# Kernel tuning notes

Measured on AMD Instinct MI355X. Metric: run time of the kernel, lower is better.

Reference implementation:

```python
import jax, jax.numpy as jnp
import numpy as np

K = 20
EPS = 1e-5


def _knn_idx(x, k):
    # x: (B, C, N) -> idx (B, N, k) of nearest neighbors (largest negative sq dist)
    xt = jnp.swapaxes(x, 1, 2)                      # (B, N, C)
    inner = -2.0 * jnp.einsum('bnc,bmc->bnm', xt, xt)
    xx = jnp.sum(x * x, axis=1)                      # (B, N)
    pd = -xx[:, :, None] - inner - xx[:, None, :]    # (B, N, N)
    return jax.lax.top_k(pd, k)[1]


def _graph_feature(x, k):
    # x: (B, C, N) -> (B, 2C, N, k): concat(neighbor - center, center)
    idx = _knn_idx(x, k)                             # (B, N, k) int
    xt = jnp.swapaxes(x, 1, 2)                       # (B, N, C)
    neigh = jax.vmap(lambda f, i: f[i])(xt, idx)     # (B, N, k, C)
    center = jnp.broadcast_to(xt[:, :, None, :], neigh.shape)
    feat = jnp.concatenate([neigh - center, center], axis=-1)  # (B, N, k, 2C)
    return jnp.transpose(feat, (0, 3, 1, 2))         # (B, 2C, N, k)


def _bn_lrelu(y, g, b, rm, rv, chan_axis_nd):
    # inference-mode batchnorm per channel (dim 1) followed by LeakyReLU(0.2)
    shp = [1, -1] + [1] * chan_axis_nd
    scale = (g / jnp.sqrt(rv + EPS)).reshape(shp)
    y = (y - rm.reshape(shp)) * scale + b.reshape(shp)
    return jnp.where(y > 0, y, 0.2 * y)


def _edge_block(x, w, g, b, rm, rv):
    f = _graph_feature(x, K)                          # (B, 2C, N, k)
    y = jnp.einsum('oc,bcnk->bonk', w, f)            # conv2d 1x1, no bias
    y = _bn_lrelu(y, g, b, rm, rv, 2)
    return jnp.max(y, axis=-1)                       # max over k -> (B, O, N)


def setup_inputs() -> dict:
    key = jax.random.key(0)
    ks = jax.random.split(key, 32)
    B, N = 8, 4096
    d = {'x': jax.random.normal(ks[0], (B, 1, N), jnp.float32)}
    wshapes = {'w1': (64, 2), 'w2': (64, 128), 'w3': (128, 128), 'w4': (256, 256),
               'w5': (1024, 512), 'wreg': (1, 1024)}
    i = 1
    for name, s in wshapes.items():
        d[name] = jax.random.normal(ks[i], s, jnp.float32) * 0.1
        i += 1
    chans = {'1': 64, '2': 64, '3': 128, '4': 256, '5': 1024}
    for tag, c in chans.items():
        d['g' + tag] = 1.0 + 0.1 * jax.random.normal(ks[i], (c,), jnp.float32); i += 1
        d['b' + tag] = 0.1 * jax.random.normal(ks[i], (c,), jnp.float32); i += 1
        d['rm' + tag] = 0.1 * jax.random.normal(ks[i], (c,), jnp.float32); i += 1
        d['rv' + tag] = jax.random.uniform(ks[i], (c,), jnp.float32, 0.5, 1.5); i += 1
    return d


def reference(x, w1, w2, w3, w4, w5, wreg,
              g1, b1, rm1, rv1, g2, b2, rm2, rv2, g3, b3, rm3, rv3,
              g4, b4, rm4, rv4, g5, b5, rm5, rv5):
    x1 = _edge_block(x, w1, g1, b1, rm1, rv1)        # (B, 64, N)
    x2 = _edge_block(x1, w2, g2, b2, rm2, rv2)       # (B, 64, N)
    x3 = _edge_block(x2, w3, g3, b3, rm3, rv3)       # (B, 128, N)
    x4 = _edge_block(x3, w4, g4, b4, rm4, rv4)       # (B, 256, N)
    h = jnp.concatenate([x1, x2, x3, x4], axis=1)    # (B, 512, N)
    h = jnp.einsum('oc,bcn->bon', w5, h)             # conv1d 1x1 -> (B, 1024, N)
    h = _bn_lrelu(h, g5, b5, rm5, rv5, 1)
    return jnp.einsum('oc,bcn->bon', wreg, h)        # (B, 1, N)
```

## Files before the change

kernel.cpp:

```cpp
#include <hip/hip_runtime.h>
#include <math.h>


constexpr int NPT = 4096;
constexpr int BATCH = 8;
constexpr int PTS = BATCH * NPT;
constexpr float EPS = 1e-5f;
#define KC 16
#define PAD 68
#define PADB 132
#define NEG_INF -3.4e38f

typedef __attribute__((ext_vector_type(8))) short bf16x8;
typedef __attribute__((ext_vector_type(4))) float f32x4;

__device__ __forceinline__ ushort f2bf(float f) {
    unsigned u = __float_as_uint(f);
    return (ushort)((u + 0x7fffu + ((u >> 16) & 1u)) >> 16);
}

__global__ __launch_bounds__(256) void sqnorm(const float* __restrict__ X,
                                              float* __restrict__ xx, int C) {
    int p = blockIdx.x * 256 + threadIdx.x;
    if (p >= PTS) return;
    float s = 0.f;
    const float* row = X + (size_t)p * C;
    for (int c = 0; c < C; ++c) s = fmaf(row[c], row[c], s);
    xx[p] = s;
}

__global__ __launch_bounds__(256) void sqnorm_cvt(const float* __restrict__ X,
                                                  float* __restrict__ xx,
                                                  ushort* __restrict__ Xh,
                                                  ushort* __restrict__ Xl, int C) {
    int p = blockIdx.x * 256 + threadIdx.x;
    if (p >= PTS) return;
    const float* row = X + (size_t)p * C;
    ushort* hr = Xh + (size_t)p * C;
    ushort* lr = Xl + (size_t)p * C;
    float s = 0.f;
    for (int c = 0; c < C; ++c) {
        float v = row[c];
        s = fmaf(v, v, s);
        ushort hb = f2bf(v);
        float hf = __uint_as_float((unsigned)hb << 16);
        hr[c] = hb;
        lr[c] = f2bf(v - hf);
    }
    xx[p] = s;
}

__global__ __launch_bounds__(256) void pd_mfma(const ushort* __restrict__ Xh,
                                               const ushort* __restrict__ Xl,
                                               const float* __restrict__ xx,
                                               float* __restrict__ pd0,
                                               int C, int bbase, size_t pdstride) {
    int b = bbase + blockIdx.y;
    float* pd = pd0 + (size_t)blockIdx.y * pdstride;
    int bid = blockIdx.x;
    int ti = 0, rem = bid;
    while (rem >= 32 - ti) { rem -= 32 - ti; ++ti; }
    int tj = ti + rem;
    int rowbase = ti * 128, colbase = tj * 128;
    int p0 = b * NPT;

    __shared__ ushort Rh[128][40], Rl[128][40], Ch[128][40], Cl[128][40];
    __shared__ float xxr[128], xxc[128];
    int tid = threadIdx.x;
    int lane = tid & 63, wid = tid >> 6;
    int wr = wid >> 1, wc = wid & 1;

    if (tid < 128) xxr[tid] = xx[p0 + rowbase + tid];
    else           xxc[tid - 128] = xx[p0 + colbase + tid - 128];

    const int pt = tid >> 1;
    const int co = (tid & 1) * 16;
    size_t rrow = (size_t)(p0 + rowbase + pt) * C;
    size_t crow = (size_t)(p0 + colbase + pt) * C;

    f32x4 z = {0.f, 0.f, 0.f, 0.f};
    f32x4 acc[4][4];
#pragma unroll
    for (int sr = 0; sr < 4; ++sr)
#pragma unroll
        for (int sc = 0; sc < 4; ++sc) acc[sr][sc] = z;

    for (int c0 = 0; c0 < C; c0 += 32) {
        uint4 vrh0 = *(const uint4*)&Xh[rrow + c0 + co];
        uint4 vrh1 = *(const uint4*)&Xh[rrow + c0 + co + 8];
        uint4 vrl0 = *(const uint4*)&Xl[rrow + c0 + co];
        uint4 vrl1 = *(const uint4*)&Xl[rrow + c0 + co + 8];
        uint4 vch0 = *(const uint4*)&Xh[crow + c0 + co];
        uint4 vch1 = *(const uint4*)&Xh[crow + c0 + co + 8];
        uint4 vcl0 = *(const uint4*)&Xl[crow + c0 + co];
        uint4 vcl1 = *(const uint4*)&Xl[crow + c0 + co + 8];
        __syncthreads();
        *(uint4*)&Rh[pt][co] = vrh0; *(uint4*)&Rh[pt][co + 8] = vrh1;
        *(uint4*)&Rl[pt][co] = vrl0; *(uint4*)&Rl[pt][co + 8] = vrl1;
        *(uint4*)&Ch[pt][co] = vch0; *(uint4*)&Ch[pt][co + 8] = vch1;
        *(uint4*)&Cl[pt][co] = vcl0; *(uint4*)&Cl[pt][co + 8] = vcl1;
        __syncthreads();
        bf16x8 ah[4], al[4], bh[4], bl[4];
#pragma unroll
        for (int s = 0; s < 4; ++s) {
            int ar = wr * 64 + s * 16 + (lane & 15);
            int br = wc * 64 + s * 16 + (lane & 15);
            int ko = (lane >> 4) * 8;
            ah[s] = *(const bf16x8*)&Rh[ar][ko];
            al[s] = *(const bf16x8*)&Rl[ar][ko];
            bh[s] = *(const bf16x8*)&Ch[br][ko];
            bl[s] = *(const bf16x8*)&Cl[br][ko];
        }
#pragma unroll
        for (int sr = 0; sr < 4; ++sr)
#pragma unroll
            for (int sc = 0; sc < 4; ++sc) {
                acc[sr][sc] = __builtin_amdgcn_mfma_f32_16x16x32_bf16(ah[sr], bh[sc], acc[sr][sc], 0, 0, 0);
                acc[sr][sc] = __builtin_amdgcn_mfma_f32_16x16x32_bf16(ah[sr], bl[sc], acc[sr][sc], 0, 0, 0);
                acc[sr][sc] = __builtin_amdgcn_mfma_f32_16x16x32_bf16(al[sr], bh[sc], acc[sr][sc], 0, 0, 0);
            }
    }

    int rl0 = wr * 64 + (lane >> 4) * 4;
    int ml  = wc * 64 + (lane & 15);
#pragma unroll
    for (int sr = 0; sr < 4; ++sr)
#pragma unroll
        for (int sc = 0; sc < 4; ++sc) {
            int mm = ml + sc * 16;
            float xm = xxc[mm];
#pragma unroll
            for (int reg = 0; reg < 4; ++reg) {
                int rr = rl0 + sr * 16 + reg;
                float o = 2.f * acc[sr][sc][reg] - xxr[rr] - xm;
                pd[(size_t)(rowbase + rr) * NPT + colbase + mm] = o;
            }
        }
    if (ti != tj) {
#pragma unroll
        for (int sr = 0; sr < 4; ++sr) {
            int rr0 = rl0 + sr * 16;
#pragma unroll
            for (int sc = 0; sc < 4; ++sc) {
                int mm = ml + sc * 16;
                float xm = xxc[mm];
                float4 o;
                o.x = 2.f * acc[sr][sc][0] - xm - xxr[rr0 + 0];
                o.y = 2.f * acc[sr][sc][1] - xm - xxr[rr0 + 1];
                o.z = 2.f * acc[sr][sc][2] - xm - xxr[rr0 + 2];
                o.w = 2.f * acc[sr][sc][3] - xm - xxr[rr0 + 3];
                *(float4*)&pd[(size_t)(colbase + mm) * NPT + rowbase + rr0] = o;
            }
        }
    }
}

__device__ __forceinline__ void topk_core(float (&v)[64], int lane, int b,
                                          int* __restrict__ op) {
    float m1 = NEG_INF, m2 = NEG_INF;
    int j1 = 0, j2 = 0;
#pragma unroll
    for (int j = 0; j < 64; ++j) {
        float vv = v[j];
        bool c1 = vv > m1;
        bool c2 = vv > m2;
        m2 = c1 ? m1 : (c2 ? vv : m2);
        j2 = c1 ? j1 : (c2 ? j : j2);
        m1 = c1 ? vv : m1;
        j1 = c1 ? j : j1;
    }
    bool have2 = true;
    unsigned long long remM = 0ull;
    for (int t = 0; t < 20; ++t) {
        int g1 = ((j1 >> 2) << 8) + (lane << 2) + (j1 & 3);
        float bv = m1; int gi = g1;
#pragma unroll
        for (int s = 1; s < 64; s <<= 1) {
            float ov = __shfl_xor(bv, s);
            int og = __shfl_xor(gi, s);
            if (ov > bv || (ov == bv && og < gi)) { bv = ov; gi = og; }
        }
        if (lane == 0) op[t] = b * NPT + gi;
        bool needscan = false;
        if (gi == g1) {
            remM |= 1ull << j1;
            if (have2) { m1 = m2; j1 = j2; have2 = false; }
            else needscan = true;
        }
        if (__any(needscan)) {
            if (needscan) {
                m1 = NEG_INF; m2 = NEG_INF; j1 = 0; j2 = 0;
#pragma unroll
                for (int j = 0; j < 64; ++j) {
                    bool alive = !((remM >> j) & 1ull);
                    float vv = alive ? v[j] : NEG_INF;
                    bool c1 = vv > m1;
                    bool c2 = vv > m2;
                    m2 = c1 ? m1 : (c2 ? vv : m2);
                    j2 = c1 ? j1 : (c2 ? j : j2);
                    m1 = c1 ? vv : m1;
                    j1 = c1 ? j : j1;
                }
                have2 = true;
            }
        }
    }
}

__global__ __launch_bounds__(256) void topk20(const float* __restrict__ pd0,
                                              int* __restrict__ idxout,
                                              int bbase, size_t pdstride) {
    int b = bbase + blockIdx.y;
    const float* pd = pd0 + (size_t)blockIdx.y * pdstride;
    int row = blockIdx.x * 4 + (threadIdx.x >> 6);
    int lane = threadIdx.x & 63;
    const float4* prow4 = (const float4*)(pd + (size_t)row * NPT);
    float v[64];
#pragma unroll
    for (int q = 0; q < 16; ++q) {
        float4 t = prow4[q * 64 + lane];
        v[q * 4 + 0] = t.x; v[q * 4 + 1] = t.y;
        v[q * 4 + 2] = t.z; v[q * 4 + 3] = t.w;
    }
    topk_core(v, lane, b, idxout + (size_t)(b * NPT + row) * 20);
}

__global__ __launch_bounds__(256) void topk1(const float* __restrict__ X,
                                             const float* __restrict__ xx,
                                             int* __restrict__ idxout) {
    int b = blockIdx.y;
    int row = blockIdx.x * 4 + (threadIdx.x >> 6);
    int lane = threadIdx.x & 63;
    int p0 = b * NPT;
    float xr = X[p0 + row];
    float xxr = xx[p0 + row];
    const float4* xb4 = (const float4*)(X + p0);
    const float4* xxb4 = (const float4*)(xx + p0);
    float v[64];
#pragma unroll
    for (int q = 0; q < 16; ++q) {
        float4 xm = xb4[q * 64 + lane];
        float4 xxm = xxb4[q * 64 + lane];
        v[q * 4 + 0] = (2.f * (xr * xm.x) - xxr) - xxm.x;
        v[q * 4 + 1] = (2.f * (xr * xm.y) - xxr) - xxm.y;
        v[q * 4 + 2] = (2.f * (xr * xm.z) - xxr) - xxm.z;
        v[q * 4 + 3] = (2.f * (xr * xm.w) - xxr) - xxm.w;
    }
    topk_core(v, lane, b, idxout + (size_t)(b * NPT + row) * 20);
}

__global__ __launch_bounds__(256) void ut1(const float* __restrict__ X,
                                           const float* __restrict__ w,
                                           float* __restrict__ U,
                                           float* __restrict__ T) {
    int p = blockIdx.x * 4 + (threadIdx.x >> 6);
    int o = threadIdx.x & 63;
    float xv = X[p];
    float wa = w[o * 2];
    float wt = w[o * 2 + 1] - wa;
    U[(size_t)p * 64 + o] = wa * xv;
    T[(size_t)p * 64 + o] = wt * xv;
}

__global__ __launch_bounds__(256) void ut_gemm(const float* __restrict__ X,
                                               const float* __restrict__ w,
                                               float* __restrict__ U,
                                               float* __restrict__ T,
                                               int C, int O) {
    __shared__ float Xs[KC][PAD];
    __shared__ float Wa[KC][PAD];
    __shared__ float Wt[KC][PAD];
    int tid = threadIdx.x;
    int tx = tid & 15;
    int ty = tid >> 4;
    int pbase = blockIdx.x * 64;
    int obase = blockIdx.y * 64;
    int lc = tid & 15;
    int li = tid >> 4;
    float aU[4][4] = {}, aT[4][4] = {};
    for (int c0 = 0; c0 < C; c0 += KC) {
        int c = c0 + lc;
#pragma unroll
        for (int r = 0; r < 4; ++r) {
            int i = li + r * 16;
            Xs[lc][i] = X[(size_t)(pbase + i) * C + c];
            const float* wrow = w + (size_t)(obase + i) * (2 * C);
            float wa = wrow[c];
            Wa[lc][i] = wa;
            Wt[lc][i] = wrow[C + c] - wa;
        }
        __syncthreads();
#pragma unroll
        for (int cc = 0; cc < KC; ++cc) {
            float xv[4], wav[4], wtv[4];
#pragma unroll
            for (int i = 0; i < 4; ++i) xv[i] = Xs[cc][tx * 4 + i];
#pragma unroll
            for (int j = 0; j < 4; ++j) { wav[j] = Wa[cc][ty * 4 + j]; wtv[j] = Wt[cc][ty * 4 + j]; }
#pragma unroll
            for (int j = 0; j < 4; ++j)
#pragma unroll
                for (int i = 0; i < 4; ++i) {
                    aU[j][i] = fmaf(wav[j], xv[i], aU[j][i]);
                    aT[j][i] = fmaf(wtv[j], xv[i], aT[j][i]);
                }
        }
        __syncthreads();
    }
#pragma unroll
    for (int j = 0; j < 4; ++j)
#pragma unroll
        for (int i = 0; i < 4; ++i) {
            size_t p = pbase + tx * 4 + i;
            int o = obase + ty * 4 + j;
            U[p * O + o] = aU[j][i];
            T[p * O + o] = aT[j][i];
        }
}

__global__ __launch_bounds__(256) void gather_max4(const float* __restrict__ U,
                                                   const float* __restrict__ T,
                                                   const int* __restrict__ idx,
                                                   const float* __restrict__ g,
                                                   const float* __restrict__ bb,
                                                   const float* __restrict__ rm,
                                                   const float* __restrict__ rv,
                                                   float* __restrict__ Xout, int O) {
    int tpp = O / 4;
    int ppb = 256 / tpp;
    int lp = threadIdx.x / tpp;
    int o4 = (threadIdx.x % tpp) * 4;
    int p = blockIdx.x * ppb + lp;
    const int* ip = idx + (size_t)p * 20;
    float4 m = {NEG_INF, NEG_INF, NEG_INF, NEG_INF};
#pragma unroll
    for (int k = 0; k < 20; ++k) {
        int j = ip[k];
        float4 u = *(const float4*)&U[(size_t)j * O + o4];
        m.x = fmaxf(m.x, u.x); m.y = fmaxf(m.y, u.y);
        m.z = fmaxf(m.z, u.z); m.w = fmaxf(m.w, u.w);
    }
    float4 t = *(const float4*)&T[(size_t)p * O + o4];
    float4 gg = *(const float4*)&g[o4];
    float4 bv = *(const float4*)&bb[o4];
    float4 rmv = *(const float4*)&rm[o4];
    float4 rvv = *(const float4*)&rv[o4];
    float4 y;
    y.x = (m.x + t.x - rmv.x) * (gg.x / sqrtf(rvv.x + EPS)) + bv.x;
    y.y = (m.y + t.y - rmv.y) * (gg.y / sqrtf(rvv.y + EPS)) + bv.y;
    y.z = (m.z + t.z - rmv.z) * (gg.z / sqrtf(rvv.z + EPS)) + bv.z;
    y.w = (m.w + t.w - rmv.w) * (gg.w / sqrtf(rvv.w + EPS)) + bv.w;
    y.x = y.x > 0.f ? y.x : 0.2f * y.x;
    y.y = y.y > 0.f ? y.y : 0.2f * y.y;
    y.z = y.z > 0.f ? y.z : 0.2f * y.z;
    y.w = y.w > 0.f ? y.w : 0.2f * y.w;
    *(float4*)&Xout[(size_t)p * O + o4] = y;
}

__global__ __launch_bounds__(256) void head_partial(const float* __restrict__ X1,
                                                    const float* __restrict__ X2,
                                                    const float* __restrict__ X3,
                                                    const float* __restrict__ X4,
                                                    const float* __restrict__ w5,
                                                    const float* __restrict__ wreg,
                                                    const float* __restrict__ g,
                                                    const float* __restrict__ bb,
                                                    const float* __restrict__ rm,
                                                    const float* __restrict__ rv,
                                                    float* __restrict__ partial) {
    __shared__ __align__(16) float Ws[KC][PADB];
    __shared__ __align__(16) float Hs[KC][PADB];
    __shared__ float red[16][PADB];
    int tid = threadIdx.x;
    int tx = tid & 15;
    int ty = tid >> 4;
    int o0 = blockIdx.x * 128;
    int p0 = blockIdx.y * 128;
    int sc4 = (tid & 3) * 4;
    int spt = tid >> 2;
    float acc[2][2][4][4] = {};
    for (int c0 = 0; c0 < 512; c0 += KC) {
        const float* src;
        int coff, Cs;
        if (c0 < 64)       { src = X1; coff = c0;       Cs = 64; }
        else if (c0 < 128) { src = X2; coff = c0 - 64;  Cs = 64; }
        else if (c0 < 256) { src = X3; coff = c0 - 128; Cs = 128; }
        else               { src = X4; coff = c0 - 256; Cs = 256; }
#pragma unroll
        for (int h = 0; h < 2; ++h) {
            int pt = spt + h * 64;
            float4 wv = *(const float4*)&w5[(size_t)(o0 + pt) * 512 + c0 + sc4];
            float4 hv = *(const float4*)&src[(size_t)(p0 + pt) * Cs + coff + sc4];
            Ws[sc4 + 0][pt] = wv.x; Ws[sc4 + 1][pt] = wv.y;
            Ws[sc4 + 2][pt] = wv.z; Ws[sc4 + 3][pt] = wv.w;
            Hs[sc4 + 0][pt] = hv.x; Hs[sc4 + 1][pt] = hv.y;
            Hs[sc4 + 2][pt] = hv.z; Hs[sc4 + 3][pt] = hv.w;
        }
        __syncthreads();
#pragma unroll
        for (int cc = 0; cc < KC; ++cc) {
            float4 a0 = *(const float4*)&Ws[cc][ty * 4];
            float4 a1 = *(const float4*)&Ws[cc][64 + ty * 4];
            float4 b0 = *(const float4*)&Hs[cc][tx * 4];
            float4 b1 = *(const float4*)&Hs[cc][64 + tx * 4];
            float ar[2][4] = {{a0.x, a0.y, a0.z, a0.w}, {a1.x, a1.y, a1.z, a1.w}};
            float br[2][4] = {{b0.x, b0.y, b0.z, b0.w}, {b1.x, b1.y, b1.z, b1.w}};
#pragma unroll
            for (int rh = 0; rh < 2; ++rh)
#pragma unroll
                for (int i = 0; i < 4; ++i)
#pragma unroll
                    for (int ch = 0; ch < 2; ++ch)
#pragma unroll
                        for (int j = 0; j < 4; ++j)
                            acc[rh][ch][i][j] = fmaf(ar[rh][i], br[ch][j], acc[rh][ch][i][j]);
        }
        __syncthreads();
    }
    float pacc[2][4] = {};
#pragma unroll
    for (int rh = 0; rh < 2; ++rh)
#pragma unroll
        for (int i = 0; i < 4; ++i) {
            int o = o0 + rh * 64 + ty * 4 + i;
            float scale = g[o] / sqrtf(rv[o] + EPS);
            float sm = rm[o], sb = bb[o], wr = wreg[o];
#pragma unroll
            for (int ch = 0; ch < 2; ++ch)
#pragma unroll
                for (int j = 0; j < 4; ++j) {
                    float y = (acc[rh][ch][i][j] - sm) * scale + sb;
                    y = y > 0.f ? y : 0.2f * y;
                    pacc[ch][j] = fmaf(wr, y, pacc[ch][j]);
                }
        }
#pragma unroll
    for (int ch = 0; ch < 2; ++ch)
#pragma unroll
        for (int j = 0; j < 4; ++j)
            red[ty][ch * 64 + tx * 4 + j] = pacc[ch][j];
    __syncthreads();
    if (tid < 128) {
        float s = 0.f;
#pragma unroll
        for (int q = 0; q < 16; ++q) s += red[q][tid];
        partial[(size_t)blockIdx.x * PTS + p0 + tid] = s;
    }
}

__global__ __launch_bounds__(256) void head_reduce(const float* __restrict__ partial,
                                                   float* __restrict__ out) {
    int p = blockIdx.x * 256 + threadIdx.x;
    if (p >= PTS) return;
    float s = 0.f;
#pragma unroll
    for (int q = 0; q < 8; ++q) s += partial[(size_t)q * PTS + p];
    out[p] = s;
}

extern "C" void kernel_launch(void* const* d_in, const int* in_sizes, int n_in,
                              void* d_out, int out_size, void* d_ws, size_t ws_size,
                              hipStream_t stream) {
    const float* x    = (const float*)d_in[0];
    const float* w1   = (const float*)d_in[1];
    const float* w2   = (const float*)d_in[2];
    const float* w3   = (const float*)d_in[3];
    const float* w4   = (const float*)d_in[4];
    const float* w5   = (const float*)d_in[5];
    const float* wreg = (const float*)d_in[6];
    const float* bn[5][4];
    for (int t = 0; t < 5; ++t)
        for (int q = 0; q < 4; ++q)
            bn[t][q] = (const float*)d_in[7 + t * 4 + q];
    float* out = (float*)d_out;

    char* ws = (char*)d_ws;
    size_t o_x1  = 0;
    size_t o_x2  = o_x1  + (size_t)PTS * 64 * 4;
    size_t o_x3  = o_x2  + (size_t)PTS * 64 * 4;
    size_t o_x4  = o_x3  + (size_t)PTS * 128 * 4;
    size_t o_idx = o_x4  + (size_t)PTS * 256 * 4;
    size_t o_xx  = o_idx + (size_t)PTS * 20 * 4;
    size_t o_pd  = o_xx  + (size_t)PTS * 4;
    size_t o_u   = o_pd;
    size_t o_t   = o_u   + (size_t)PTS * 256 * 4;
    size_t pdslab = (size_t)NPT * NPT * 4;
    (void)o_t;

    float* X1 = (float*)(ws + o_x1);
    float* X2 = (float*)(ws + o_x2);
    float* X3 = (float*)(ws + o_x3);
    float* X4 = (float*)(ws + o_x4);
    int*   IDX = (int*)(ws + o_idx);
    float* XX = (float*)(ws + o_xx);
    float* PD = (float*)(ws + o_pd);
    float* U  = (float*)(ws + o_u);
    float* T  = (float*)(ws + o_u + (size_t)PTS * 256 * 4);
    float* PART = (float*)(ws + o_idx);
    ushort* XH = (ushort*)(ws + o_x4);
    ushort* XL = (ushort*)(ws + o_x4 + (size_t)PTS * 128 * 2);

    const bool pair = ws_size >= o_pd + 2 * pdslab;
    const int bstep = pair ? 2 : 1;
    const size_t pdstride = pair ? (size_t)NPT * NPT : 0;

    auto knn_layer = [&](int C) {
        for (int b = 0; b < BATCH; b += bstep) {
            pd_mfma<<<dim3(528, bstep), 256, 0, stream>>>(XH, XL, XX, PD, C, b, pdstride);
            topk20<<<dim3(NPT / 4, bstep), 256, 0, stream>>>(PD, IDX, b, pdstride);
        }
    };

    sqnorm<<<PTS / 256, 256, 0, stream>>>(x, XX, 1);
    topk1<<<dim3(NPT / 4, BATCH), 256, 0, stream>>>(x, XX, IDX);
    ut1<<<PTS / 4, 256, 0, stream>>>(x, w1, U, T);
    gather_max4<<<PTS * 16 / 256, 256, 0, stream>>>(U, T, IDX,
            bn[0][0], bn[0][1], bn[0][2], bn[0][3], X1, 64);

    sqnorm_cvt<<<PTS / 256, 256, 0, stream>>>(X1, XX, XH, XL, 64);
    knn_layer(64);
    ut_gemm<<<dim3(PTS / 64, 1), 256, 0, stream>>>(X1, w2, U, T, 64, 64);
    gather_max4<<<PTS * 16 / 256, 256, 0, stream>>>(U, T, IDX,
            bn[1][0], bn[1][1], bn[1][2], bn[1][3], X2, 64);

    sqnorm_cvt<<<PTS / 256, 256, 0, stream>>>(X2, XX, XH, XL, 64);
    knn_layer(64);
    ut_gemm<<<dim3(PTS / 64, 2), 256, 0, stream>>>(X2, w3, U, T, 64, 128);
    gather_max4<<<PTS * 32 / 256, 256, 0, stream>>>(U, T, IDX,
            bn[2][0], bn[2][1], bn[2][2], bn[2][3], X3, 128);

    sqnorm_cvt<<<PTS / 256, 256, 0, stream>>>(X3, XX, XH, XL, 128);
    knn_layer(128);
    ut_gemm<<<dim3(PTS / 64, 4), 256, 0, stream>>>(X3, w4, U, T, 128, 256);
    gather_max4<<<PTS * 64 / 256, 256, 0, stream>>>(U, T, IDX,
            bn[3][0], bn[3][1], bn[3][2], bn[3][3], X4, 256);

    head_partial<<<dim3(8, PTS / 128), 256, 0, stream>>>(X1, X2, X3, X4, w5, wreg,
            bn[4][0], bn[4][1], bn[4][2], bn[4][3], PART);
    head_reduce<<<PTS / 256, 256, 0, stream>>>(PART, out);
}
```

Baseline: 2.407 ms.

## Run head conv1d GEMM on bf16 MFMA with hi/lo split precision

Replaces the fp32 FMA tiled GEMM in the head (w5 × concatenated features) with a bf16 MFMA kernel. Both operands are split into high and low bf16 parts, and four MFMAs per tile keep near-fp32 accuracy. A small kernel pre-converts w5 into hi/lo bf16 in the workspace, and the features are converted on the fly while staging into shared memory. BN, LeakyReLU and the wreg projection are fused in the epilogue, with a wave shuffle reduction. The cost is four times the MFMA work and a small loss of precision compared with exact fp32.

```diff
diff --git a/kernel.cpp b/kernel.cpp
--- a/kernel.cpp
+++ b/kernel.cpp
@@ -8,7 +8,6 @@
 constexpr float EPS = 1e-5f;
 #define KC 16
 #define PAD 68
-#define PADB 132
 #define NEG_INF -3.4e38f
 
 typedef __attribute__((ext_vector_type(8))) short bf16x8;
@@ -17,6 +16,9 @@
 __device__ __forceinline__ ushort f2bf(float f) {
     unsigned u = __float_as_uint(f);
     return (ushort)((u + 0x7fffu + ((u >> 16) & 1u)) >> 16);
+}
+__device__ __forceinline__ unsigned pack2(ushort a, ushort b) {
+    return (unsigned)a | ((unsigned)b << 16);
 }
 
 __global__ __launch_bounds__(256) void sqnorm(const float* __restrict__ X,
@@ -48,6 +50,22 @@
         lr[c] = f2bf(v - hf);
     }
     xx[p] = s;
+}
+
+__global__ __launch_bounds__(256) void w5cvt(const float* __restrict__ w5,
+                                             ushort* __restrict__ wh,
+                                             ushort* __restrict__ wl) {
+    int i = blockIdx.x * 256 + threadIdx.x;
+    int e = i * 4;
+    float4 v = *(const float4*)&w5[e];
+    float vv[4] = {v.x, v.y, v.z, v.w};
+#pragma unroll
+    for (int q = 0; q < 4; ++q) {
+        ushort hb = f2bf(vv[q]);
+        float hf = __uint_as_float((unsigned)hb << 16);
+        wh[e + q] = hb;
+        wl[e + q] = f2bf(vv[q] - hf);
+    }
 }
 
 __global__ __launch_bounds__(256) void pd_mfma(const ushort* __restrict__ Xh,
@@ -357,95 +375,128 @@
     *(float4*)&Xout[(size_t)p * O + o4] = y;
 }
 
-__global__ __launch_bounds__(256) void head_partial(const float* __restrict__ X1,
-                                                    const float* __restrict__ X2,
-                                                    const float* __restrict__ X3,
-                                                    const float* __restrict__ X4,
-                                                    const float* __restrict__ w5,
-                                                    const float* __restrict__ wreg,
-                                                    const float* __restrict__ g,
-                                                    const float* __restrict__ bb,
-                                                    const float* __restrict__ rm,
-                                                    const float* __restrict__ rv,
-                                                    float* __restrict__ partial) {
-    __shared__ __align__(16) float Ws[KC][PADB];
-    __shared__ __align__(16) float Hs[KC][PADB];
-    __shared__ float red[16][PADB];
+__global__ __launch_bounds__(256) void head_mfma(const float* __restrict__ X1,
+                                                 const float* __restrict__ X2,
+                                                 const float* __restrict__ X3,
+                                                 const float* __restrict__ X4,
+                                                 const ushort* __restrict__ w5h,
+                                                 const ushort* __restrict__ w5l,
+                                                 const float* __restrict__ wreg,
+                                                 const float* __restrict__ g,
+                                                 const float* __restrict__ bb,
+                                                 const float* __restrict__ rm,
+                                                 const float* __restrict__ rv,
+                                                 float* __restrict__ partial) {
+    __shared__ ushort Hh[128][40], Hl[128][40], Wh[128][40], Wl[128][40];
+    __shared__ float sscale[128], srm[128], sbb[128], swreg[128];
+    __shared__ float red[2][128];
     int tid = threadIdx.x;
-    int tx = tid & 15;
-    int ty = tid >> 4;
+    int lane = tid & 63, wid = tid >> 6;
+    int wr = wid >> 1, wc = wid & 1;
     int o0 = blockIdx.x * 128;
     int p0 = blockIdx.y * 128;
-    int sc4 = (tid & 3) * 4;
-    int spt = tid >> 2;
-    float acc[2][2][4][4] = {};
-    for (int c0 = 0; c0 < 512; c0 += KC) {
+
+    if (tid < 128) {
+        int o = o0 + tid;
+        sscale[tid] = g[o] / sqrtf(rv[o] + EPS);
+        srm[tid] = rm[o]; sbb[tid] = bb[o]; swreg[tid] = wreg[o];
+    }
+
+    const int pt = tid >> 1;
+    const int co = (tid & 1) * 16;
+
+    f32x4 z = {0.f, 0.f, 0.f, 0.f};
+    f32x4 acc[4][4];
+#pragma unroll
+    for (int sr = 0; sr < 4; ++sr)
+#pragma unroll
+        for (int sc = 0; sc < 4; ++sc) acc[sr][sc] = z;
+
+    for (int c0 = 0; c0 < 512; c0 += 32) {
         const float* src;
         int coff, Cs;
         if (c0 < 64)       { src = X1; coff = c0;       Cs = 64; }
         else if (c0 < 128) { src = X2; coff = c0 - 64;  Cs = 64; }
         else if (c0 < 256) { src = X3; coff = c0 - 128; Cs = 128; }
         else               { src = X4; coff = c0 - 256; Cs = 256; }
-#pragma unroll
-        for (int h = 0; h < 2; ++h) {
-            int pt = spt + h * 64;
-            float4 wv = *(const float4*)&w5[(size_t)(o0 + pt) * 512 + c0 + sc4];
-            float4 hv = *(const float4*)&src[(size_t)(p0 + pt) * Cs + coff + sc4];
-            Ws[sc4 + 0][pt] = wv.x; Ws[sc4 + 1][pt] = wv.y;
-            Ws[sc4 + 2][pt] = wv.z; Ws[sc4 + 3][pt] = wv.w;
-            Hs[sc4 + 0][pt] = hv.x; Hs[sc4 + 1][pt] = hv.y;
-            Hs[sc4 + 2][pt] = hv.z; Hs[sc4 + 3][pt] = hv.w;
-        }
+        const float* hp = &src[(size_t)(p0 + pt) * Cs + coff + co];
+        float4 f0 = *(const float4*)&hp[0];
+        float4 f1 = *(const float4*)&hp[4];
+        float4 f2 = *(const float4*)&hp[8];
+        float4 f3 = *(const float4*)&hp[12];
+        size_t wrow = (size_t)(o0 + pt) * 512 + c0 + co;
+        uint4 wh0 = *(const uint4*)&w5h[wrow];
+        uint4 wh1 = *(const uint4*)&w5h[wrow + 8];
+        uint4 wl0 = *(const uint4*)&w5l[wrow];
+        uint4 wl1 = *(const uint4*)&w5l[wrow + 8];
+        float hv[16] = {f0.x, f0.y, f0.z, f0.w, f1.x, f1.y, f1.z, f1.w,
+                        f2.x, f2.y, f2.z, f2.w, f3.x, f3.y, f3.z, f3.w};
+        ushort hb[16], lb[16];
+#pragma unroll
+        for (int q = 0; q < 16; ++q) {
+            hb[q] = f2bf(hv[q]);
+            float hf = __uint_as_float((unsigned)hb[q] << 16);
+            lb[q] = f2bf(hv[q] - hf);
+        }
+        uint4 hh0 = {pack2(hb[0], hb[1]), pack2(hb[2], hb[3]), pack2(hb[4], hb[5]), pack2(hb[6], hb[7])};
+        uint4 hh1 = {pack2(hb[8], hb[9]), pack2(hb[10], hb[11]), pack2(hb[12], hb[13]), pack2(hb[14], hb[15])};
+        uint4 hl0 = {pack2(lb[0], lb[1]), pack2(lb[2], lb[3]), pack2(lb[4], lb[5]), pack2(lb[6], lb[7])};
+        uint4 hl1 = {pack2(lb[8], lb[9]), pack2(lb[10], lb[11]), pack2(lb[12], lb[13]), pack2(lb[14], lb[15])};
         __syncthreads();
-#pragma unroll
-        for (int cc = 0; cc < KC; ++cc) {
-            float4 a0 = *(const float4*)&Ws[cc][ty * 4];
-            float4 a1 = *(const float4*)&Ws[cc][64 + ty * 4];
-            float4 b0 = *(const float4*)&Hs[cc][tx * 4];
-            float4 b1 = *(const float4*)&Hs[cc][64 + tx * 4];
-            float ar[2][4] = {{a0.x, a0.y, a0.z, a0.w}, {a1.x, a1.y, a1.z, a1.w}};
-            float br[2][4] = {{b0.x, b0.y, b0.z, b0.w}, {b1.x, b1.y, b1.z, b1.w}};
-#pragma unroll
-            for (int rh = 0; rh < 2; ++rh)
-#pragma unroll
-                for (int i = 0; i < 4; ++i)
-#pragma unroll
-                    for (int ch = 0; ch < 2; ++ch)
-#pragma unroll
-                        for (int j = 0; j < 4; ++j)
-                            acc[rh][ch][i][j] = fmaf(ar[rh][i], br[ch][j], acc[rh][ch][i][j]);
-        }
+        *(uint4*)&Hh[pt][co] = hh0; *(uint4*)&Hh[pt][co + 8] = hh1;
+        *(uint4*)&Hl[pt][co] = hl0; *(uint4*)&Hl[pt][co + 8] = hl1;
+        *(uint4*)&Wh[pt][co] = wh0; *(uint4*)&Wh[pt][co + 8] = wh1;
+        *(uint4*)&Wl[pt][co] = wl0; *(uint4*)&Wl[pt][co + 8] = wl1;
         __syncthreads();
-    }
-    float pacc[2][4] = {};
-#pragma unroll
-    for (int rh = 0; rh < 2; ++rh)
-#pragma unroll
-        for (int i = 0; i < 4; ++i) {
-            int o = o0 + rh * 64 + ty * 4 + i;
-            float scale = g[o] / sqrtf(rv[o] + EPS);
-            float sm = rm[o], sb = bb[o], wr = wreg[o];
-#pragma unroll
-            for (int ch = 0; ch < 2; ++ch)
-#pragma unroll
-                for (int j = 0; j < 4; ++j) {
-                    float y = (acc[rh][ch][i][j] - sm) * scale + sb;
-                    y = y > 0.f ? y : 0.2f * y;
-                    pacc[ch][j] = fmaf(wr, y, pacc[ch][j]);
-                }
-        }
-#pragma unroll
-    for (int ch = 0; ch < 2; ++ch)
-#pragma unroll
-        for (int j = 0; j < 4; ++j)
-            red[ty][ch * 64 + tx * 4 + j] = pacc[ch][j];
+        bf16x8 ah[4], al[4], bh[4], bl[4];
+#pragma unroll
+        for (int s = 0; s < 4; ++s) {
+            int orow = wr * 64 + s * 16 + (lane & 15);
+            int prow = wc * 64 + s * 16 + (lane & 15);
+            int ko = (lane >> 4) * 8;
+            ah[s] = *(const bf16x8*)&Wh[orow][ko];
+            al[s] = *(const bf16x8*)&Wl[orow][ko];
+            bh[s] = *(const bf16x8*)&Hh[prow][ko];
+            bl[s] = *(const bf16x8*)&Hl[prow][ko];
+        }
+#pragma unroll
+        for (int sr = 0; sr < 4; ++sr)
+#pragma unroll
+            for (int sc = 0; sc < 4; ++sc) {
+                acc[sr][sc] = __builtin_amdgcn_mfma_f32_16x16x32_bf16(ah[sr], bh[sc], acc[sr][sc], 0, 0, 0);
+                acc[sr][sc] = __builtin_amdgcn_mfma_f32_16x16x32_bf16(ah[sr], bl[sc], acc[sr][sc], 0, 0, 0);
+                acc[sr][sc] = __builtin_amdgcn_mfma_f32_16x16x32_bf16(al[sr], bh[sc], acc[sr][sc], 0, 0, 0);
+                acc[sr][sc] = __builtin_amdgcn_mfma_f32_16x16x32_bf16(al[sr], bl[sc], acc[sr][sc], 0, 0, 0);
+            }
+    }
+
+    float psum[4] = {0.f, 0.f, 0.f, 0.f};
+#pragma unroll
+    for (int sr = 0; sr < 4; ++sr)
+#pragma unroll
+        for (int reg = 0; reg < 4; ++reg) {
+            int ol = wr * 64 + sr * 16 + (lane >> 4) * 4 + reg;
+            float scale = sscale[ol], smv = srm[ol], sbv = sbb[ol], wrv = swreg[ol];
+#pragma unroll
+            for (int sc = 0; sc < 4; ++sc) {
+                float y = (acc[sr][sc][reg] - smv) * scale + sbv;
+                y = y > 0.f ? y : 0.2f * y;
+                psum[sc] = fmaf(wrv, y, psum[sc]);
+            }
+        }
+#pragma unroll
+    for (int sc = 0; sc < 4; ++sc) {
+        psum[sc] += __shfl_xor(psum[sc], 16);
+        psum[sc] += __shfl_xor(psum[sc], 32);
+    }
+    if ((lane >> 4) == 0) {
+#pragma unroll
+        for (int sc = 0; sc < 4; ++sc)
+            red[wr][wc * 64 + sc * 16 + lane] = psum[sc];
+    }
     __syncthreads();
-    if (tid < 128) {
-        float s = 0.f;
-#pragma unroll
-        for (int q = 0; q < 16; ++q) s += red[q][tid];
-        partial[(size_t)blockIdx.x * PTS + p0 + tid] = s;
-    }
+    if (tid < 128)
+        partial[(size_t)blockIdx.x * PTS + p0 + tid] = red[0][tid] + red[1][tid];
 }
 
 __global__ __launch_bounds__(256) void head_reduce(const float* __restrict__ partial,
@@ -483,9 +534,7 @@
     size_t o_xx  = o_idx + (size_t)PTS * 20 * 4;
     size_t o_pd  = o_xx  + (size_t)PTS * 4;
     size_t o_u   = o_pd;
-    size_t o_t   = o_u   + (size_t)PTS * 256 * 4;
     size_t pdslab = (size_t)NPT * NPT * 4;
-    (void)o_t;
 
     float* X1 = (float*)(ws + o_x1);
     float* X2 = (float*)(ws + o_x2);
@@ -499,6 +548,8 @@
     float* PART = (float*)(ws + o_idx);
     ushort* XH = (ushort*)(ws + o_x4);
     ushort* XL = (ushort*)(ws + o_x4 + (size_t)PTS * 128 * 2);
+    ushort* W5H = (ushort*)(ws + o_u);
+    ushort* W5L = W5H + (size_t)1024 * 512;
 
     const bool pair = ws_size >= o_pd + 2 * pdslab;
     const int bstep = pair ? 2 : 1;
@@ -535,7 +586,8 @@
     gather_max4<<<PTS * 64 / 256, 256, 0, stream>>>(U, T, IDX,
             bn[3][0], bn[3][1], bn[3][2], bn[3][3], X4, 256);
 
-    head_partial<<<dim3(8, PTS / 128), 256, 0, stream>>>(X1, X2, X3, X4, w5, wreg,
-            bn[4][0], bn[4][1], bn[4][2], bn[4][3], PART);
+    w5cvt<<<512, 256, 0, stream>>>(w5, W5H, W5L);
+    head_mfma<<<dim3(8, PTS / 128), 256, 0, stream>>>(X1, X2, X3, X4, W5H, W5L,
+            wreg, bn[4][0], bn[4][1], bn[4][2], bn[4][3], PART);
     head_reduce<<<PTS / 256, 256, 0, stream>>>(PART, out);
 }
```

Result: faster. 2.155 ms, median of 2 (-10.5%).
